# Optimization experiments

Hardware: AMD Instinct MI355X
Metric: run time of the kernel (lower is better)

The kernel has to match this reference:

```python
import jax, jax.numpy as jnp
import numpy as np

B, L, D = 1024, 30, 300   # batch, title length, total_dim
H, HD = 20, 20            # num_heads, head_dim
VOCAB = 30000


def _xavier_uniform(key, shape):
    # torch nn.init.xavier_uniform_ on a 3D tensor [H, din, dout*]:
    # fan_in = size(1) * prod(size(2:)), fan_out = size(0) * prod(size(2:))
    receptive = int(np.prod(shape[2:])) if len(shape) > 2 else 1
    fan_in = shape[1] * receptive
    fan_out = shape[0] * receptive
    bound = float(np.sqrt(6.0 / (fan_in + fan_out)))
    return jax.random.uniform(key, shape, jnp.float32, -bound, bound)


def setup_inputs() -> dict:
    key = jax.random.key(0)
    k_y, k_seq, k_q, k_v = jax.random.split(key, 4)
    y = jax.random.normal(k_y, (B, L, D), jnp.float32)
    seq = jax.random.randint(k_seq, (B, L), 0, VOCAB, jnp.int64)
    Q = _xavier_uniform(k_q, (H, D, D))
    V = _xavier_uniform(k_v, (H, D, HD))
    return {"y": y, "sequences_input_title": seq, "Q": Q, "V": V}


def reference(y, sequences_input_title, Q, V):
    # mask over key positions: [B, 1, 1, L]
    mask = (sequences_input_title > 0).astype(y.dtype)[:, None, None, :]
    # per-head query projection: [B, H, L, D]
    a1 = jnp.einsum('bld,hde->bhle', y, Q)
    # raw scores: [B, H, L, L]
    a2 = jnp.einsum('bhle,bme->bhlm', a1, y)
    a3 = jnp.exp(a2)  # NOTE: no max-subtraction, faithful to source
    # denominator uses masked scores, numerator does NOT (faithful bug-for-bug)
    a5 = jnp.sum(a3 * mask, axis=-1, keepdims=True) + 1e-6
    alpha = a3 / a5
    # weighted values then per-head output projection
    h0 = jnp.einsum('bhlm,bmd->bhld', alpha, y)
    h1 = jnp.einsum('bhld,hdf->bhlf', h0, V)     # [B, H, L, HD]
    # concat heads along last dim (head-major blocks, matching torch.cat)
    return h1.transpose(0, 2, 1, 3).reshape(y.shape[0], y.shape[1], -1)
```

## Files before the change

kernel.cpp:

```cpp
#include <hip/hip_runtime.h>
#include <hip/hip_bf16.h>
#include <math.h>

#define Bb 1024
#define Ll 30
#define Dd 300
#define Hh 20
#define HDd 20

typedef __attribute__((ext_vector_type(8))) short short8;
typedef __attribute__((ext_vector_type(4))) float f32x4;
typedef __attribute__((ext_vector_type(4))) unsigned short u16x4;

#define SW(row, col) ((row)*320 + ((((col) >> 3) ^ ((row) & 7)) << 3) + ((col) & 7))

#define QELEMS (Hh*19*10*64*8)
#define VELEMS (Hh*2*10*64*8)
#define WS_NEEDED ((size_t)(2*QELEMS + 2*VELEMS) * 2)

__device__ __forceinline__ unsigned short cvt_hi(float x) {
    return __builtin_bit_cast(unsigned short, __float2bfloat16(x));
}
__device__ __forceinline__ void splitc(float x, unsigned short& h, unsigned short& l) {
    h = cvt_hi(x);
    float hf = __uint_as_float((unsigned)h << 16);
    l = cvt_hi(x - hf);
}
__device__ __forceinline__ void bf16split(float x, unsigned short& h, unsigned short& l) {
    unsigned u = __float_as_uint(x);
    unsigned hr = (u + 0x7FFFu + ((u >> 16) & 1u)) >> 16;
    float hf = __uint_as_float(hr << 16);
    float r = x - hf;
    unsigned v = __float_as_uint(r);
    unsigned lr = (v + 0x7FFFu + ((v >> 16) & 1u)) >> 16;
    h = (unsigned short)hr; l = (unsigned short)lr;
}

__global__ void pack_q(const float* __restrict__ Q,
                       unsigned short* __restrict__ qh, unsigned short* __restrict__ ql) {
    int g = blockIdx.x * blockDim.x + threadIdx.x;
    if (g >= Hh*19*10*64) return;
    int l = g & 63;
    int t = g >> 6;
    int ks = t % 10; t /= 10;
    int nt = t % 19; int h = t / 19;
    int e = 16*nt + (l & 15);
    int kbase = 32*ks + 8*(l >> 4);
    unsigned hp[4], lp[4];
    #pragma unroll
    for (int p = 0; p < 4; ++p) {
        int k0 = kbase + 2*p, k1 = k0 + 1;
        float x0 = (k0 < Dd && e < Dd) ? Q[h*Dd*Dd + k0*Dd + e] : 0.f;
        float x1 = (k1 < Dd && e < Dd) ? Q[h*Dd*Dd + k1*Dd + e] : 0.f;
        unsigned short h0,l0,h1,l1;
        bf16split(x0,h0,l0); bf16split(x1,h1,l1);
        hp[p] = (unsigned)h0 | ((unsigned)h1 << 16);
        lp[p] = (unsigned)l0 | ((unsigned)l1 << 16);
    }
    ((uint4*)qh)[g] = make_uint4(hp[0],hp[1],hp[2],hp[3]);
    ((uint4*)ql)[g] = make_uint4(lp[0],lp[1],lp[2],lp[3]);
}

__global__ void pack_v(const float* __restrict__ V,
                       unsigned short* __restrict__ vh, unsigned short* __restrict__ vl) {
    int g = blockIdx.x * blockDim.x + threadIdx.x;
    if (g >= Hh*2*10*64) return;
    int l = g & 63;
    int t = g >> 6;
    int ks = t % 10; t /= 10;
    int nt = t % 2; int h = t / 2;
    int f = 16*nt + (l & 15);
    int kbase = 32*ks + 8*(l >> 4);
    unsigned hp[4], lp[4];
    #pragma unroll
    for (int p = 0; p < 4; ++p) {
        int k0 = kbase + 2*p, k1 = k0 + 1;
        float x0 = (k0 < Dd && f < HDd) ? V[h*Dd*HDd + k0*HDd + f] : 0.f;
        float x1 = (k1 < Dd && f < HDd) ? V[h*Dd*HDd + k1*HDd + f] : 0.f;
        unsigned short h0,l0,h1,l1;
        bf16split(x0,h0,l0); bf16split(x1,h1,l1);
        hp[p] = (unsigned)h0 | ((unsigned)h1 << 16);
        lp[p] = (unsigned)l0 | ((unsigned)l1 << 16);
    }
    ((uint4*)vh)[g] = make_uint4(hp[0],hp[1],hp[2],hp[3]);
    ((uint4*)vl)[g] = make_uint4(lp[0],lp[1],lp[2],lp[3]);
}

__global__ __launch_bounds__(512, 2)
void mha_v5(const float* __restrict__ y, const int* __restrict__ seq,
            const unsigned short* __restrict__ qh, const unsigned short* __restrict__ ql,
            const unsigned short* __restrict__ vh, const unsigned short* __restrict__ vl,
            float* __restrict__ out)
{
    __shared__ __align__(16) unsigned short y_h[32*320], y_l[32*320];
    __shared__ __align__(16) unsigned short a1h[32*320], a1l[32*320];

    const int bid = blockIdx.x;
    const int h = bid >> 10, b = bid & 1023;
    const int tid = threadIdx.x;
    const int lane = tid & 63, wid = tid >> 6;
    const int lrow = lane & 15, lk = lane >> 4;
    const int l7 = lrow & 7;

    const float* yb = y + (size_t)b * (Ll * Dd);
    const float4 z4 = make_float4(0.f, 0.f, 0.f, 0.f);
    for (int idx4 = tid; idx4 < 32*80; idx4 += 512) {
        int row = idx4 / 80;
        int c4  = (idx4 - row*80) << 2;
        float4 v = (row < Ll && c4 < Dd) ? *reinterpret_cast<const float4*>(yb + row*Dd + c4) : z4;
        unsigned short h0, l0, h1, l1, h2, l2, h3, l3;
        splitc(v.x, h0, l0);
        splitc(v.y, h1, l1);
        splitc(v.z, h2, l2);
        splitc(v.w, h3, l3);
        u16x4 hv, lv;
        hv[0] = h0; hv[1] = h1; hv[2] = h2; hv[3] = h3;
        lv[0] = l0; lv[1] = l1; lv[2] = l2; lv[3] = l3;
        int sidx = SW(row, c4);
        *reinterpret_cast<u16x4*>(&y_h[sidx]) = hv;
        *reinterpret_cast<u16x4*>(&y_l[sidx]) = lv;
    }
    if (tid < 128) {
        int r = tid & 31, c = 38 + ((tid >> 5) & 1);
        unsigned short* p = (tid >> 6) ? a1l : a1h;
        int sc = c ^ (r & 7);
        *((uint4*)&p[r*320 + sc*8]) = make_uint4(0,0,0,0);
    }
    __syncthreads();

    for (int ht = wid; ht < 38; ht += 8) {
        const int nt = ht >> 1, Mt = ht & 1;
        f32x4 acc0 = (f32x4){0,0,0,0}, acc1 = (f32x4){0,0,0,0};
        const unsigned short* qhp = qh + (size_t)((h*19 + nt)*10)*512 + lane*8;
        const unsigned short* qlp = ql + (size_t)((h*19 + nt)*10)*512 + lane*8;
        const int arow = (16*Mt + lrow)*320;
        #pragma unroll
        for (int ks = 0; ks < 10; ++ks) {
            short8 bh = *(const short8*)(qhp + ks*512);
            short8 bl = *(const short8*)(qlp + ks*512);
            const int ia = arow + (((4*ks + lk) ^ l7) << 3);
            short8 ah = *(const short8*)&y_h[ia];
            short8 al = *(const short8*)&y_l[ia];
            if (ks & 1) {
                acc1 = __builtin_amdgcn_mfma_f32_16x16x32_bf16(ah, bh, acc1, 0,0,0);
                acc1 = __builtin_amdgcn_mfma_f32_16x16x32_bf16(al, bh, acc1, 0,0,0);
                acc1 = __builtin_amdgcn_mfma_f32_16x16x32_bf16(ah, bl, acc1, 0,0,0);
            } else {
                acc0 = __builtin_amdgcn_mfma_f32_16x16x32_bf16(ah, bh, acc0, 0,0,0);
                acc0 = __builtin_amdgcn_mfma_f32_16x16x32_bf16(al, bh, acc0, 0,0,0);
                acc0 = __builtin_amdgcn_mfma_f32_16x16x32_bf16(ah, bl, acc0, 0,0,0);
            }
        }
        f32x4 a = acc0 + acc1;
        const int col = 16*nt + lrow;
        #pragma unroll
        for (int r = 0; r < 4; ++r) {
            int row = 16*Mt + 4*lk + r;
            unsigned short hv, lv; splitc(a[r], hv, lv);
            int sidx = SW(row, col);
            a1h[sidx] = hv;
            a1l[sidx] = lv;
        }
    }
    __syncthreads();

    f32x4 Pacc = (f32x4){0,0,0,0};
    float alf[2][4];

    if (wid < 2) {
        const int Mt = wid;
        f32x4 acc[2][2];
        #pragma unroll
        for (int i = 0; i < 2; ++i) { acc[i][0] = (f32x4){0,0,0,0}; acc[i][1] = (f32x4){0,0,0,0}; }
        const int arow = (16*Mt + lrow)*320;
        #pragma unroll
        for (int ntp = 0; ntp < 10; ++ntp) {
            const int ch = ((4*ntp + lk) ^ l7) << 3;
            short8 ah = *(const short8*)&a1h[arow + ch];
            short8 al = *(const short8*)&a1l[arow + ch];
            #pragma unroll
            for (int Nt = 0; Nt < 2; ++Nt) {
                int ib = (16*Nt + lrow)*320 + ch;
                short8 bh = *(const short8*)&y_h[ib];
                short8 bl = *(const short8*)&y_l[ib];
                acc[Nt][ntp&1] = __builtin_amdgcn_mfma_f32_16x16x32_bf16(ah, bh, acc[Nt][ntp&1], 0,0,0);
                acc[Nt][ntp&1] = __builtin_amdgcn_mfma_f32_16x16x32_bf16(al, bh, acc[Nt][ntp&1], 0,0,0);
                acc[Nt][ntp&1] = __builtin_amdgcn_mfma_f32_16x16x32_bf16(ah, bl, acc[Nt][ntp&1], 0,0,0);
            }
        }
        f32x4 S0 = acc[0][0] + acc[0][1];
        f32x4 S1 = acc[1][0] + acc[1][1];
        const float mk0 = (seq[b*Ll + lrow] > 0) ? 1.f : 0.f;
        const float mk1 = (lrow < 14) ? ((seq[b*Ll + 16 + lrow] > 0) ? 1.f : 0.f) : 0.f;
        #pragma unroll
        for (int r = 0; r < 4; ++r) {
            float s0 = S0[r], s1 = S1[r];
            float v = fmaxf(s0, (lrow < 14) ? s1 : -3.4e38f);
            #pragma unroll
            for (int off = 8; off >= 1; off >>= 1)
                v = fmaxf(v, __shfl_xor(v, off, 64));
            float e0 = __expf(s0 - v);
            float e1 = __expf(s1 - v);
            float sum = e0 * mk0 + e1 * mk1;
            #pragma unroll
            for (int off = 8; off >= 1; off >>= 1)
                sum += __shfl_xor(sum, off, 64);
            float denom = sum + 1e-6f * __expf(-v);
            alf[0][r] = e0 / denom;
            alf[1][r] = (lrow < 14) ? e1 / denom : 0.f;
        }
    } else if (wid < 6) {
        const int w = wid - 2, Mtp = w >> 1, Ntp = w & 1;
        f32x4 acc0 = (f32x4){0,0,0,0}, acc1 = (f32x4){0,0,0,0};
        const unsigned short* vhp = vh + (size_t)((h*2 + Ntp)*10)*512 + lane*8;
        const unsigned short* vlp = vl + (size_t)((h*2 + Ntp)*10)*512 + lane*8;
        const int arow = (16*Mtp + lrow)*320;
        #pragma unroll
        for (int ks = 0; ks < 10; ++ks) {
            short8 bh = *(const short8*)(vhp + ks*512);
            short8 bl = *(const short8*)(vlp + ks*512);
            int ia = arow + (((4*ks + lk) ^ l7) << 3);
            short8 ah = *(const short8*)&y_h[ia];
            short8 al = *(const short8*)&y_l[ia];
            if (ks & 1) {
                acc1 = __builtin_amdgcn_mfma_f32_16x16x32_bf16(ah, bh, acc1, 0,0,0);
                acc1 = __builtin_amdgcn_mfma_f32_16x16x32_bf16(al, bh, acc1, 0,0,0);
                acc1 = __builtin_amdgcn_mfma_f32_16x16x32_bf16(ah, bl, acc1, 0,0,0);
            } else {
                acc0 = __builtin_amdgcn_mfma_f32_16x16x32_bf16(ah, bh, acc0, 0,0,0);
                acc0 = __builtin_amdgcn_mfma_f32_16x16x32_bf16(al, bh, acc0, 0,0,0);
                acc0 = __builtin_amdgcn_mfma_f32_16x16x32_bf16(ah, bl, acc0, 0,0,0);
            }
        }
        Pacc = acc0 + acc1;
    }
    __syncthreads();

    if (wid < 2) {
        const int Mt = wid;
        #pragma unroll
        for (int Nt = 0; Nt < 2; ++Nt)
            #pragma unroll
            for (int r = 0; r < 4; ++r)
                a1l[SW(16*Mt + 4*lk + r, 16*Nt + lrow)] = cvt_hi(alf[Nt][r]);
    } else if (wid < 6) {
        const int w = wid - 2, Mtp = w >> 1, Ntp = w & 1;
        #pragma unroll
        for (int r = 0; r < 4; ++r)
            a1h[SW(16*Ntp + lrow, 16*Mtp + 4*lk + r)] = cvt_hi(Pacc[r]);
    }
    __syncthreads();

    if (wid < 4) {
        const int Mt = wid >> 1, Nt = wid & 1;
        short8 af = *(const short8*)&a1l[(16*Mt + lrow)*320 + ((lk ^ l7) << 3)];
        short8 pf = *(const short8*)&a1h[(16*Nt + lrow)*320 + ((lk ^ l7) << 3)];
        f32x4 O = __builtin_amdgcn_mfma_f32_16x16x32_bf16(af, pf, (f32x4){0,0,0,0}, 0,0,0);
        #pragma unroll
        for (int r = 0; r < 4; ++r) {
            int q = 16*Mt + 4*lk + r;
            int f = 16*Nt + lrow;
            if (q < Ll && f < HDd)
                out[(size_t)b*(Ll*Hh*HDd) + q*(Hh*HDd) + h*HDd + f] = O[r];
        }
    }
}

__global__ __launch_bounds__(256, 3)
void mha_fused_fp32(const float* __restrict__ y,
                    const int* __restrict__ seq,
                    const float* __restrict__ Q,
                    const float* __restrict__ V,
                    float* __restrict__ out)
{
    __shared__ float ys[32][320];
    __shared__ float alphaS[32][33];
    __shared__ float Plds[32][20];
    __shared__ float maskSf[32];

    const int bid = blockIdx.x;
    const int h = bid >> 10;
    const int b = bid & 1023;
    const int tid = threadIdx.x;
    const int tj = tid & 31;
    const int ti = tid >> 5;
    const int r0 = ti * 4;

    const float* yb = y + b * (Ll * Dd);
    for (int i = tid; i < 32 * 320; i += 256) {
        int row = i / 320;
        int col = i - row * 320;
        float v = 0.f;
        if (row < Ll && col < Dd) v = yb[row * Dd + col];
        ys[row][col] = v;
    }
    if (tid < 32) {
        float m = 0.f;
        if (tid < Ll) m = (seq[b * Ll + tid] > 0) ? 1.f : 0.f;
        maskSf[tid] = m;
    }
    __syncthreads();

    float a1reg[4][10];
    #pragma unroll
    for (int r = 0; r < 4; ++r)
        #pragma unroll
        for (int k = 0; k < 10; ++k) a1reg[r][k] = 0.f;

    const float* Qh = Q + h * (Dd * Dd) + tj;
    for (int d0 = 0; d0 < Dd; d0 += 4) {
        float ysv[4][4];
        #pragma unroll
        for (int r = 0; r < 4; ++r) {
            float4 t = *reinterpret_cast<const float4*>(&ys[r0 + r][d0]);
            ysv[r][0] = t.x; ysv[r][1] = t.y; ysv[r][2] = t.z; ysv[r][3] = t.w;
        }
        #pragma unroll
        for (int dd = 0; dd < 4; ++dd) {
            const float* qp = Qh + (d0 + dd) * Dd;
            float qv[10];
            #pragma unroll
            for (int k = 0; k < 9; ++k) qv[k] = qp[32 * k];
            qv[9] = (tj < 12) ? qp[288] : 0.f;
            #pragma unroll
            for (int r = 0; r < 4; ++r) {
                float yd = ysv[r][dd];
                #pragma unroll
                for (int k = 0; k < 10; ++k)
                    a1reg[r][k] = fmaf(yd, qv[k], a1reg[r][k]);
            }
        }
    }

    float Sreg[4] = {0.f, 0.f, 0.f, 0.f};
    for (int m = 0; m < Ll; ++m) {
        float yv[10];
        #pragma unroll
        for (int k = 0; k < 10; ++k) yv[k] = ys[m][tj + 32 * k];
        float part[4];
        #pragma unroll
        for (int r = 0; r < 4; ++r) {
            float s = 0.f;
            #pragma unroll
            for (int k = 0; k < 10; ++k) s = fmaf(a1reg[r][k], yv[k], s);
            part[r] = s;
        }
        #pragma unroll
        for (int off = 16; off >= 1; off >>= 1)
            #pragma unroll
            for (int r = 0; r < 4; ++r)
                part[r] += __shfl_xor(part[r], off, 64);
        #pragma unroll
        for (int r = 0; r < 4; ++r)
            if (tj == m) Sreg[r] = part[r];
    }

    const float maskv = maskSf[tj];
    float Areg[4];
    #pragma unroll
    for (int r = 0; r < 4; ++r) {
        float v = (tj < Ll) ? Sreg[r] : -3.4e38f;
        #pragma unroll
        for (int off = 16; off >= 1; off >>= 1)
            v = fmaxf(v, __shfl_xor(v, off, 64));
        float e = __expf(Sreg[r] - v);
        float s = (tj < Ll) ? e * maskv : 0.f;
        #pragma unroll
        for (int off = 16; off >= 1; off >>= 1)
            s += __shfl_xor(s, off, 64);
        float denom = s + 1e-6f * __expf(-v);
        Areg[r] = e / denom;
    }
    #pragma unroll
    for (int r = 0; r < 4; ++r)
        if (r0 + r < Ll && tj < Ll) alphaS[r0 + r][tj] = Areg[r];

    float Pacc[4] = {0.f, 0.f, 0.f, 0.f};
    if (tj < HDd) {
        const float* Vh = V + h * (Dd * HDd) + tj;
        for (int d0 = 0; d0 < Dd; d0 += 4) {
            float ysv[4][4];
            #pragma unroll
            for (int r = 0; r < 4; ++r) {
                float4 t = *reinterpret_cast<const float4*>(&ys[r0 + r][d0]);
                ysv[r][0] = t.x; ysv[r][1] = t.y; ysv[r][2] = t.z; ysv[r][3] = t.w;
            }
            float vv[4];
            #pragma unroll
            for (int dd = 0; dd < 4; ++dd) vv[dd] = Vh[(d0 + dd) * HDd];
            #pragma unroll
            for (int r = 0; r < 4; ++r)
                #pragma unroll
                for (int dd = 0; dd < 4; ++dd)
                    Pacc[r] = fmaf(ysv[r][dd], vv[dd], Pacc[r]);
        }
    }
    #pragma unroll
    for (int r = 0; r < 4; ++r)
        if (tj < HDd && r0 + r < Ll) Plds[r0 + r][tj] = Pacc[r];
    __syncthreads();

    float* outb = out + b * (Ll * Hh * HDd) + h * HDd;
    for (int t = tid; t < Ll * HDd; t += 256) {
        int l = t / HDd;
        int f = t - l * HDd;
        float acc = 0.f;
        #pragma unroll
        for (int m = 0; m < Ll; ++m)
            acc = fmaf(alphaS[l][m], Plds[m][f], acc);
        outb[l * (Hh * HDd) + f] = acc;
    }
}

extern "C" void kernel_launch(void* const* d_in, const int* in_sizes, int n_in,
                              void* d_out, int out_size, void* d_ws, size_t ws_size,
                              hipStream_t stream) {
    (void)in_sizes; (void)n_in; (void)out_size;
    const float* y   = (const float*)d_in[0];
    const int*   seq = (const int*)d_in[1];
    const float* Q   = (const float*)d_in[2];
    const float* V   = (const float*)d_in[3];
    float* out = (float*)d_out;

    if (ws_size < WS_NEEDED) {
        hipLaunchKernelGGL(mha_fused_fp32, dim3(Bb * Hh), dim3(256), 0, stream, y, seq, Q, V, out);
        return;
    }

    unsigned short* qh = (unsigned short*)d_ws;
    unsigned short* ql = qh + QELEMS;
    unsigned short* vh = ql + QELEMS;
    unsigned short* vl = vh + VELEMS;

    pack_q<<<dim3((Hh*19*10*64 + 255)/256), dim3(256), 0, stream>>>(Q, qh, ql);
    pack_v<<<dim3((Hh*2*10*64 + 255)/256), dim3(256), 0, stream>>>(V, vh, vl);
    mha_v5<<<dim3(Bb * Hh), dim3(512), 0, stream>>>(y, seq, qh, ql, vh, vl, out);
}
```

Before: 708.3 us.

## Fold V projection into Q-projection work loop and break MFMA dependency chains

The P = y·V tiles move out of the phase after the scores and into the Q-projection work loop, now 42 items spread over 8 waves with a rotated slot so waves 4-7 take the extra work. This removes one phase in which only 6 of 8 waves were busy. Each work item now loads all 10 Q/V fragments from global memory into registers up front, and it splits the accumulators 6 ways so the three MFMAs per k-step no longer depend on each other. This raises register pressure under launch_bounds(512,2), which could cause spills or lower occupancy.

```diff
diff --git a/kernel.cpp b/kernel.cpp
--- a/kernel.cpp
+++ b/kernel.cpp
@@ -87,7 +87,7 @@
 }
 
 __global__ __launch_bounds__(512, 2)
-void mha_v5(const float* __restrict__ y, const int* __restrict__ seq,
+void mha_v6(const float* __restrict__ y, const int* __restrict__ seq,
             const unsigned short* __restrict__ qh, const unsigned short* __restrict__ ql,
             const unsigned short* __restrict__ vh, const unsigned short* __restrict__ vl,
             float* __restrict__ out)
@@ -128,68 +128,109 @@
     }
     __syncthreads();
 
-    for (int ht = wid; ht < 38; ht += 8) {
-        const int nt = ht >> 1, Mt = ht & 1;
-        f32x4 acc0 = (f32x4){0,0,0,0}, acc1 = (f32x4){0,0,0,0};
-        const unsigned short* qhp = qh + (size_t)((h*19 + nt)*10)*512 + lane*8;
-        const unsigned short* qlp = ql + (size_t)((h*19 + nt)*10)*512 + lane*8;
-        const int arow = (16*Mt + lrow)*320;
-        #pragma unroll
-        for (int ks = 0; ks < 10; ++ks) {
-            short8 bh = *(const short8*)(qhp + ks*512);
-            short8 bl = *(const short8*)(qlp + ks*512);
-            const int ia = arow + (((4*ks + lk) ^ l7) << 3);
-            short8 ah = *(const short8*)&y_h[ia];
-            short8 al = *(const short8*)&y_l[ia];
-            if (ks & 1) {
-                acc1 = __builtin_amdgcn_mfma_f32_16x16x32_bf16(ah, bh, acc1, 0,0,0);
-                acc1 = __builtin_amdgcn_mfma_f32_16x16x32_bf16(al, bh, acc1, 0,0,0);
-                acc1 = __builtin_amdgcn_mfma_f32_16x16x32_bf16(ah, bl, acc1, 0,0,0);
-            } else {
-                acc0 = __builtin_amdgcn_mfma_f32_16x16x32_bf16(ah, bh, acc0, 0,0,0);
-                acc0 = __builtin_amdgcn_mfma_f32_16x16x32_bf16(al, bh, acc0, 0,0,0);
-                acc0 = __builtin_amdgcn_mfma_f32_16x16x32_bf16(ah, bl, acc0, 0,0,0);
-            }
-        }
-        f32x4 a = acc0 + acc1;
-        const int col = 16*nt + lrow;
-        #pragma unroll
-        for (int r = 0; r < 4; ++r) {
-            int row = 16*Mt + 4*lk + r;
-            unsigned short hv, lv; splitc(a[r], hv, lv);
-            int sidx = SW(row, col);
-            a1h[sidx] = hv;
-            a1l[sidx] = lv;
-        }
-    }
-    __syncthreads();
-
+    const int wslot = (wid + 4) & 7;
+    bool hasP = false; int pMt = 0, pNt = 0;
     f32x4 Pacc = (f32x4){0,0,0,0};
+
+    for (int it = wslot; it < 42; it += 8) {
+        if (it < 38) {
+            const int nt = it >> 1, Mt = it & 1;
+            const unsigned short* qhp = qh + (size_t)((h*19 + nt)*10)*512 + lane*8;
+            const unsigned short* qlp = ql + (size_t)((h*19 + nt)*10)*512 + lane*8;
+            short8 qhr[10], qlr[10];
+            #pragma unroll
+            for (int ks = 0; ks < 10; ++ks) {
+                qhr[ks] = *(const short8*)(qhp + ks*512);
+                qlr[ks] = *(const short8*)(qlp + ks*512);
+            }
+            f32x4 acc[2][3];
+            #pragma unroll
+            for (int i = 0; i < 2; ++i)
+                #pragma unroll
+                for (int j = 0; j < 3; ++j) acc[i][j] = (f32x4){0,0,0,0};
+            const int arow = (16*Mt + lrow)*320;
+            #pragma unroll
+            for (int ks = 0; ks < 10; ++ks) {
+                const int ia = arow + (((4*ks + lk) ^ l7) << 3);
+                short8 ah = *(const short8*)&y_h[ia];
+                short8 al = *(const short8*)&y_l[ia];
+                const int p = ks & 1;
+                acc[p][0] = __builtin_amdgcn_mfma_f32_16x16x32_bf16(ah, qhr[ks], acc[p][0], 0,0,0);
+                acc[p][1] = __builtin_amdgcn_mfma_f32_16x16x32_bf16(al, qhr[ks], acc[p][1], 0,0,0);
+                acc[p][2] = __builtin_amdgcn_mfma_f32_16x16x32_bf16(ah, qlr[ks], acc[p][2], 0,0,0);
+            }
+            f32x4 a = ((acc[0][0] + acc[1][0]) + (acc[0][1] + acc[1][1])) + (acc[0][2] + acc[1][2]);
+            const int col = 16*nt + lrow;
+            #pragma unroll
+            for (int r = 0; r < 4; ++r) {
+                int row = 16*Mt + 4*lk + r;
+                unsigned short hv, lv; splitc(a[r], hv, lv);
+                int sidx = SW(row, col);
+                a1h[sidx] = hv;
+                a1l[sidx] = lv;
+            }
+        } else {
+            const int pi = it - 38;
+            const int Mtp = pi >> 1, Ntp = pi & 1;
+            const unsigned short* vhp = vh + (size_t)((h*2 + Ntp)*10)*512 + lane*8;
+            const unsigned short* vlp = vl + (size_t)((h*2 + Ntp)*10)*512 + lane*8;
+            short8 vhr[10], vlr[10];
+            #pragma unroll
+            for (int ks = 0; ks < 10; ++ks) {
+                vhr[ks] = *(const short8*)(vhp + ks*512);
+                vlr[ks] = *(const short8*)(vlp + ks*512);
+            }
+            f32x4 acc[2][3];
+            #pragma unroll
+            for (int i = 0; i < 2; ++i)
+                #pragma unroll
+                for (int j = 0; j < 3; ++j) acc[i][j] = (f32x4){0,0,0,0};
+            const int arow = (16*Mtp + lrow)*320;
+            #pragma unroll
+            for (int ks = 0; ks < 10; ++ks) {
+                const int ia = arow + (((4*ks + lk) ^ l7) << 3);
+                short8 ah = *(const short8*)&y_h[ia];
+                short8 al = *(const short8*)&y_l[ia];
+                const int p = ks & 1;
+                acc[p][0] = __builtin_amdgcn_mfma_f32_16x16x32_bf16(ah, vhr[ks], acc[p][0], 0,0,0);
+                acc[p][1] = __builtin_amdgcn_mfma_f32_16x16x32_bf16(al, vhr[ks], acc[p][1], 0,0,0);
+                acc[p][2] = __builtin_amdgcn_mfma_f32_16x16x32_bf16(ah, vlr[ks], acc[p][2], 0,0,0);
+            }
+            Pacc = ((acc[0][0] + acc[1][0]) + (acc[0][1] + acc[1][1])) + (acc[0][2] + acc[1][2]);
+            hasP = true; pMt = Mtp; pNt = Ntp;
+        }
+    }
+    __syncthreads();
+
     float alf[2][4];
-
     if (wid < 2) {
         const int Mt = wid;
-        f32x4 acc[2][2];
-        #pragma unroll
-        for (int i = 0; i < 2; ++i) { acc[i][0] = (f32x4){0,0,0,0}; acc[i][1] = (f32x4){0,0,0,0}; }
+        f32x4 acc[2][2][3];
+        #pragma unroll
+        for (int i = 0; i < 2; ++i)
+            #pragma unroll
+            for (int j = 0; j < 2; ++j)
+                #pragma unroll
+                for (int k = 0; k < 3; ++k) acc[i][j][k] = (f32x4){0,0,0,0};
         const int arow = (16*Mt + lrow)*320;
         #pragma unroll
         for (int ntp = 0; ntp < 10; ++ntp) {
             const int ch = ((4*ntp + lk) ^ l7) << 3;
             short8 ah = *(const short8*)&a1h[arow + ch];
             short8 al = *(const short8*)&a1l[arow + ch];
+            const int p = ntp & 1;
             #pragma unroll
             for (int Nt = 0; Nt < 2; ++Nt) {
                 int ib = (16*Nt + lrow)*320 + ch;
                 short8 bh = *(const short8*)&y_h[ib];
                 short8 bl = *(const short8*)&y_l[ib];
-                acc[Nt][ntp&1] = __builtin_amdgcn_mfma_f32_16x16x32_bf16(ah, bh, acc[Nt][ntp&1], 0,0,0);
-                acc[Nt][ntp&1] = __builtin_amdgcn_mfma_f32_16x16x32_bf16(al, bh, acc[Nt][ntp&1], 0,0,0);
-                acc[Nt][ntp&1] = __builtin_amdgcn_mfma_f32_16x16x32_bf16(ah, bl, acc[Nt][ntp&1], 0,0,0);
-            }
-        }
-        f32x4 S0 = acc[0][0] + acc[0][1];
-        f32x4 S1 = acc[1][0] + acc[1][1];
+                acc[Nt][p][0] = __builtin_amdgcn_mfma_f32_16x16x32_bf16(ah, bh, acc[Nt][p][0], 0,0,0);
+                acc[Nt][p][1] = __builtin_amdgcn_mfma_f32_16x16x32_bf16(al, bh, acc[Nt][p][1], 0,0,0);
+                acc[Nt][p][2] = __builtin_amdgcn_mfma_f32_16x16x32_bf16(ah, bl, acc[Nt][p][2], 0,0,0);
+            }
+        }
+        f32x4 S0 = ((acc[0][0][0] + acc[0][1][0]) + (acc[0][0][1] + acc[0][1][1])) + (acc[0][0][2] + acc[0][1][2]);
+        f32x4 S1 = ((acc[1][0][0] + acc[1][1][0]) + (acc[1][0][1] + acc[1][1][1])) + (acc[1][0][2] + acc[1][1][2]);
         const float mk0 = (seq[b*Ll + lrow] > 0) ? 1.f : 0.f;
         const float mk1 = (lrow < 14) ? ((seq[b*Ll + 16 + lrow] > 0) ? 1.f : 0.f) : 0.f;
         #pragma unroll
@@ -209,30 +250,6 @@
             alf[0][r] = e0 / denom;
             alf[1][r] = (lrow < 14) ? e1 / denom : 0.f;
         }
-    } else if (wid < 6) {
-        const int w = wid - 2, Mtp = w >> 1, Ntp = w & 1;
-        f32x4 acc0 = (f32x4){0,0,0,0}, acc1 = (f32x4){0,0,0,0};
-        const unsigned short* vhp = vh + (size_t)((h*2 + Ntp)*10)*512 + lane*8;
-        const unsigned short* vlp = vl + (size_t)((h*2 + Ntp)*10)*512 + lane*8;
-        const int arow = (16*Mtp + lrow)*320;
-        #pragma unroll
-        for (int ks = 0; ks < 10; ++ks) {
-            short8 bh = *(const short8*)(vhp + ks*512);
-            short8 bl = *(const short8*)(vlp + ks*512);
-            int ia = arow + (((4*ks + lk) ^ l7) << 3);
-            short8 ah = *(const short8*)&y_h[ia];
-            short8 al = *(const short8*)&y_l[ia];
-            if (ks & 1) {
-                acc1 = __builtin_amdgcn_mfma_f32_16x16x32_bf16(ah, bh, acc1, 0,0,0);
-                acc1 = __builtin_amdgcn_mfma_f32_16x16x32_bf16(al, bh, acc1, 0,0,0);
-                acc1 = __builtin_amdgcn_mfma_f32_16x16x32_bf16(ah, bl, acc1, 0,0,0);
-            } else {
-                acc0 = __builtin_amdgcn_mfma_f32_16x16x32_bf16(ah, bh, acc0, 0,0,0);
-                acc0 = __builtin_amdgcn_mfma_f32_16x16x32_bf16(al, bh, acc0, 0,0,0);
-                acc0 = __builtin_amdgcn_mfma_f32_16x16x32_bf16(ah, bl, acc0, 0,0,0);
-            }
-        }
-        Pacc = acc0 + acc1;
     }
     __syncthreads();
 
@@ -243,11 +260,11 @@
             #pragma unroll
             for (int r = 0; r < 4; ++r)
                 a1l[SW(16*Mt + 4*lk + r, 16*Nt + lrow)] = cvt_hi(alf[Nt][r]);
-    } else if (wid < 6) {
-        const int w = wid - 2, Mtp = w >> 1, Ntp = w & 1;
+    }
+    if (hasP) {
         #pragma unroll
         for (int r = 0; r < 4; ++r)
-            a1h[SW(16*Ntp + lrow, 16*Mtp + 4*lk + r)] = cvt_hi(Pacc[r]);
+            a1h[SW(16*pNt + lrow, 16*pMt + 4*lk + r)] = cvt_hi(Pacc[r]);
     }
     __syncthreads();
 
@@ -434,5 +451,5 @@
 
     pack_q<<<dim3((Hh*19*10*64 + 255)/256), dim3(256), 0, stream>>>(Q, qh, ql);
     pack_v<<<dim3((Hh*2*10*64 + 255)/256), dim3(256), 0, stream>>>(V, vh, vl);
-    mha_v5<<<dim3(Bb * Hh), dim3(512), 0, stream>>>(y, seq, qh, ql, vh, vl, out);
-}
+    mha_v6<<<dim3(Bb * Hh), dim3(512), 0, stream>>>(y, seq, qh, ql, vh, vl, out);
+}
```

Measured after the change: 1.041 ms. 46.9% more time.

## Spread score GEMM across four waves and stage scores through shared memory

Applied to the files above, without the earlier changes.

The score computation (a1·y^T) moves from two waves, each doing both N tiles, to four waves doing one 16x16 tile each. The V-projection now runs on waves 4-7 instead of 2-5. Scores are written to shared memory as hi/lo bf16 pairs and read back by two waves for the softmax. This shortens the critical path of the score phase but adds a barrier and an LDS round trip. The score written back to LDS as a bf16 hi/lo pair may lose a little precision compared with keeping it in fp32 registers.

```diff
diff --git a/kernel.cpp b/kernel.cpp
--- a/kernel.cpp
+++ b/kernel.cpp
@@ -87,10 +87,10 @@
 }
 
 __global__ __launch_bounds__(512, 2)
-void mha_v5(const float* __restrict__ y, const int* __restrict__ seq,
-            const unsigned short* __restrict__ qh, const unsigned short* __restrict__ ql,
-            const unsigned short* __restrict__ vh, const unsigned short* __restrict__ vl,
-            float* __restrict__ out)
+void mha_v10(const float* __restrict__ y, const int* __restrict__ seq,
+             const unsigned short* __restrict__ qh, const unsigned short* __restrict__ ql,
+             const unsigned short* __restrict__ vh, const unsigned short* __restrict__ vl,
+             float* __restrict__ out)
 {
     __shared__ __align__(16) unsigned short y_h[32*320], y_l[32*320];
     __shared__ __align__(16) unsigned short a1h[32*320], a1l[32*320];
@@ -164,53 +164,34 @@
     }
     __syncthreads();
 
+    f32x4 Sq = (f32x4){0,0,0,0};
     f32x4 Pacc = (f32x4){0,0,0,0};
-    float alf[2][4];
-
-    if (wid < 2) {
-        const int Mt = wid;
-        f32x4 acc[2][2];
-        #pragma unroll
-        for (int i = 0; i < 2; ++i) { acc[i][0] = (f32x4){0,0,0,0}; acc[i][1] = (f32x4){0,0,0,0}; }
+
+    if (wid < 4) {
+        const int Mt = wid >> 1, Nt = wid & 1;
+        f32x4 acc0 = (f32x4){0,0,0,0}, acc1 = (f32x4){0,0,0,0};
         const int arow = (16*Mt + lrow)*320;
+        const int brow = (16*Nt + lrow)*320;
         #pragma unroll
         for (int ntp = 0; ntp < 10; ++ntp) {
             const int ch = ((4*ntp + lk) ^ l7) << 3;
             short8 ah = *(const short8*)&a1h[arow + ch];
             short8 al = *(const short8*)&a1l[arow + ch];
-            #pragma unroll
-            for (int Nt = 0; Nt < 2; ++Nt) {
-                int ib = (16*Nt + lrow)*320 + ch;
-                short8 bh = *(const short8*)&y_h[ib];
-                short8 bl = *(const short8*)&y_l[ib];
-                acc[Nt][ntp&1] = __builtin_amdgcn_mfma_f32_16x16x32_bf16(ah, bh, acc[Nt][ntp&1], 0,0,0);
-                acc[Nt][ntp&1] = __builtin_amdgcn_mfma_f32_16x16x32_bf16(al, bh, acc[Nt][ntp&1], 0,0,0);
-                acc[Nt][ntp&1] = __builtin_amdgcn_mfma_f32_16x16x32_bf16(ah, bl, acc[Nt][ntp&1], 0,0,0);
+            short8 bh = *(const short8*)&y_h[brow + ch];
+            short8 bl = *(const short8*)&y_l[brow + ch];
+            if (ntp & 1) {
+                acc1 = __builtin_amdgcn_mfma_f32_16x16x32_bf16(ah, bh, acc1, 0,0,0);
+                acc1 = __builtin_amdgcn_mfma_f32_16x16x32_bf16(al, bh, acc1, 0,0,0);
+                acc1 = __builtin_amdgcn_mfma_f32_16x16x32_bf16(ah, bl, acc1, 0,0,0);
+            } else {
+                acc0 = __builtin_amdgcn_mfma_f32_16x16x32_bf16(ah, bh, acc0, 0,0,0);
+                acc0 = __builtin_amdgcn_mfma_f32_16x16x32_bf16(al, bh, acc0, 0,0,0);
+                acc0 = __builtin_amdgcn_mfma_f32_16x16x32_bf16(ah, bl, acc0, 0,0,0);
             }
         }
-        f32x4 S0 = acc[0][0] + acc[0][1];
-        f32x4 S1 = acc[1][0] + acc[1][1];
-        const float mk0 = (seq[b*Ll + lrow] > 0) ? 1.f : 0.f;
-        const float mk1 = (lrow < 14) ? ((seq[b*Ll + 16 + lrow] > 0) ? 1.f : 0.f) : 0.f;
-        #pragma unroll
-        for (int r = 0; r < 4; ++r) {
-            float s0 = S0[r], s1 = S1[r];
-            float v = fmaxf(s0, (lrow < 14) ? s1 : -3.4e38f);
-            #pragma unroll
-            for (int off = 8; off >= 1; off >>= 1)
-                v = fmaxf(v, __shfl_xor(v, off, 64));
-            float e0 = __expf(s0 - v);
-            float e1 = __expf(s1 - v);
-            float sum = e0 * mk0 + e1 * mk1;
-            #pragma unroll
-            for (int off = 8; off >= 1; off >>= 1)
-                sum += __shfl_xor(sum, off, 64);
-            float denom = sum + 1e-6f * __expf(-v);
-            alf[0][r] = e0 / denom;
-            alf[1][r] = (lrow < 14) ? e1 / denom : 0.f;
-        }
-    } else if (wid < 6) {
-        const int w = wid - 2, Mtp = w >> 1, Ntp = w & 1;
+        Sq = acc0 + acc1;
+    } else {
+        const int w = wid - 4, Mtp = w >> 1, Ntp = w & 1;
         f32x4 acc0 = (f32x4){0,0,0,0}, acc1 = (f32x4){0,0,0,0};
         const unsigned short* vhp = vh + (size_t)((h*2 + Ntp)*10)*512 + lane*8;
         const unsigned short* vlp = vl + (size_t)((h*2 + Ntp)*10)*512 + lane*8;
@@ -236,18 +217,55 @@
     }
     __syncthreads();
 
+    if (wid < 4) {
+        const int Mt = wid >> 1, Nt = wid & 1;
+        #pragma unroll
+        for (int r = 0; r < 4; ++r) {
+            int row = 16*Mt + 4*lk + r;
+            unsigned short hv, lv; splitc(Sq[r], hv, lv);
+            int sidx = SW(row, 64 + 16*Nt + lrow);
+            a1h[sidx] = hv;
+            a1l[sidx] = lv;
+        }
+    } else {
+        const int w = wid - 4, Mtp = w >> 1, Ntp = w & 1;
+        #pragma unroll
+        for (int r = 0; r < 4; ++r)
+            a1h[SW(16*Ntp + lrow, 16*Mtp + 4*lk + r)] = cvt_hi(Pacc[r]);
+    }
+    __syncthreads();
+
     if (wid < 2) {
         const int Mt = wid;
+        const float mk0 = (seq[b*Ll + lrow] > 0) ? 1.f : 0.f;
+        const float mk1 = (lrow < 14) ? ((seq[b*Ll + 16 + lrow] > 0) ? 1.f : 0.f) : 0.f;
+        float alf[2][4];
+        #pragma unroll
+        for (int r = 0; r < 4; ++r) {
+            int row = 16*Mt + 4*lk + r;
+            int i0 = SW(row, 64 + lrow);
+            int i1 = SW(row, 80 + lrow);
+            float s0 = __uint_as_float((unsigned)a1h[i0] << 16) + __uint_as_float((unsigned)a1l[i0] << 16);
+            float s1 = __uint_as_float((unsigned)a1h[i1] << 16) + __uint_as_float((unsigned)a1l[i1] << 16);
+            float v = fmaxf(s0, (lrow < 14) ? s1 : -3.4e38f);
+            #pragma unroll
+            for (int off = 8; off >= 1; off >>= 1)
+                v = fmaxf(v, __shfl_xor(v, off, 64));
+            float e0 = __expf(s0 - v);
+            float e1 = __expf(s1 - v);
+            float sum = e0 * mk0 + e1 * mk1;
+            #pragma unroll
+            for (int off = 8; off >= 1; off >>= 1)
+                sum += __shfl_xor(sum, off, 64);
+            float denom = sum + 1e-6f * __expf(-v);
+            alf[0][r] = e0 / denom;
+            alf[1][r] = (lrow < 14) ? e1 / denom : 0.f;
+        }
         #pragma unroll
         for (int Nt = 0; Nt < 2; ++Nt)
             #pragma unroll
             for (int r = 0; r < 4; ++r)
                 a1l[SW(16*Mt + 4*lk + r, 16*Nt + lrow)] = cvt_hi(alf[Nt][r]);
-    } else if (wid < 6) {
-        const int w = wid - 2, Mtp = w >> 1, Ntp = w & 1;
-        #pragma unroll
-        for (int r = 0; r < 4; ++r)
-            a1h[SW(16*Ntp + lrow, 16*Mtp + 4*lk + r)] = cvt_hi(Pacc[r]);
     }
     __syncthreads();
 
@@ -434,5 +452,5 @@
 
     pack_q<<<dim3((Hh*19*10*64 + 255)/256), dim3(256), 0, stream>>>(Q, qh, ql);
     pack_v<<<dim3((Hh*2*10*64 + 255)/256), dim3(256), 0, stream>>>(V, vh, vl);
-    mha_v5<<<dim3(Bb * Hh), dim3(512), 0, stream>>>(y, seq, qh, ql, vh, vl, out);
-}
+    mha_v10<<<dim3(Bb * Hh), dim3(512), 0, stream>>>(y, seq, qh, ql, vh, vl, out);
+}
```

Result: no change. 706.6 us (-0.2%).
